# Performance work log

Measured on AMD Instinct MI355X. Metric: run time of the kernel, lower is better.

## Reference

```python
import jax, jax.numpy as jnp
import numpy as np

B, S, D, H, DFF = 2, 2048, 768, 12, 3072
DH = D // H
EPS = 1e-5


def _ln(x, g, b):
    m = jnp.mean(x, axis=-1, keepdims=True)
    v = jnp.mean((x - m) ** 2, axis=-1, keepdims=True)
    return (x - m) * jax.lax.rsqrt(v + EPS) * g + b


def setup_inputs() -> dict:
    key = jax.random.key(0)
    ks = jax.random.split(key, 13)
    sd = 1.0 / np.sqrt(D)
    sf = 1.0 / np.sqrt(DFF)
    return {
        "x": jax.random.normal(ks[0], (B, S, D), jnp.float32),
        "Wq": jax.random.uniform(ks[1], (D, D), jnp.float32, -sd, sd),
        "bq": jnp.zeros((D,), jnp.float32),
        "Wk": jax.random.uniform(ks[2], (D, D), jnp.float32, -sd, sd),
        "bk": jnp.zeros((D,), jnp.float32),
        "Wv": jax.random.uniform(ks[3], (D, D), jnp.float32, -sd, sd),
        "bv": jnp.zeros((D,), jnp.float32),
        "Wo": jax.random.uniform(ks[4], (D, D), jnp.float32, -sd, sd),
        "bo": jnp.zeros((D,), jnp.float32),
        "W1": jax.random.uniform(ks[5], (D, DFF), jnp.float32, -sd, sd),
        "b1": jnp.zeros((DFF,), jnp.float32),
        "W2": jax.random.uniform(ks[6], (DFF, D), jnp.float32, -sf, sf),
        "b2": jnp.zeros((D,), jnp.float32),
        "g1": jnp.ones((D,), jnp.float32),
        "be1": jnp.zeros((D,), jnp.float32),
        "g2": jnp.ones((D,), jnp.float32),
        "be2": jnp.zeros((D,), jnp.float32),
    }


def reference(x, Wq, bq, Wk, bk, Wv, bv, Wo, bo, W1, b1, W2, b2, g1, be1, g2, be2):
    # QKV projections, then split heads: [B,S,D] -> [B,H,S,DH]
    def heads(t):
        return t.reshape(B, S, H, DH).transpose(0, 2, 1, 3)
    Q = heads(x @ Wq + bq)
    K = heads(x @ Wk + bk)
    V = heads(x @ Wv + bv)
    # Per-head loop in original == batched-over-heads attention here (same math)
    scores = jnp.einsum("bhqd,bhkd->bhqk", Q, K) / np.sqrt(DH)
    attn = jax.nn.softmax(scores, axis=-1)  # [B,H,S,S] -- dominant intermediate
    ctx = jnp.einsum("bhqk,bhkd->bhqd", attn, V)
    ctx = ctx.transpose(0, 2, 1, 3).reshape(B, S, D)  # concat heads
    x = x + (ctx @ Wo + bo)
    x = _ln(x, g1, be1)
    ffn = (jax.nn.gelu(x @ W1 + b1, approximate=False)) @ W2 + b2
    x = _ln(x + ffn, g2, be2)
    return x
```

## Files before the change

### kernel.cpp

```cpp
#include <hip/hip_runtime.h>
#include <math.h>

#define BB 2
#define SS 2048
#define DD 768
#define HH 12
#define DHH 64
#define DFFN 3072
#define MTOK (BB*SS)
#define KVSPL 4

typedef __attribute__((ext_vector_type(8))) __bf16 bf16x8;
typedef __attribute__((ext_vector_type(4))) float f32x4;
typedef __attribute__((ext_vector_type(16))) float f32x16;

__device__ __forceinline__ unsigned short f2bf(float f) {
    unsigned int b = __builtin_bit_cast(unsigned int, f);
    b += 0x7FFFu + ((b >> 16) & 1u);
    return (unsigned short)(b >> 16);
}
__device__ __forceinline__ float bf2f(unsigned short u) {
    unsigned int b = ((unsigned int)u) << 16;
    return __builtin_bit_cast(float, b);
}

__device__ __forceinline__ void gload_lds16(const void* g, void* l) {
    __builtin_amdgcn_global_load_lds((const __attribute__((address_space(1))) unsigned int*)g,
                                     (__attribute__((address_space(3))) unsigned int*)l,
                                     16, 0, 0);
}

#if __has_builtin(__builtin_amdgcn_permlane32_swap)
#define HAVE_PSWAP 1
__device__ __forceinline__ void pswap(unsigned int x, unsigned int y,
                                      unsigned int& r0, unsigned int& r1) {
    auto r = __builtin_amdgcn_permlane32_swap(x, y, false, false);
    r0 = r[0]; r1 = r[1];
}
#else
#define HAVE_PSWAP 0
__device__ __forceinline__ void pswap(unsigned int x, unsigned int y,
                                      unsigned int& r0, unsigned int& r1) {
    unsigned int xs = __shfl_xor(x, 32);
    unsigned int ys = __shfl_xor(y, 32);
    bool hi = (threadIdx.x & 32) != 0;
    r0 = hi ? ys : x;
    r1 = hi ? y : xs;
}
#endif

__device__ __forceinline__ float xhalf_max(float v) {
    unsigned int u = __builtin_bit_cast(unsigned int, v);
    unsigned int a, b;
    pswap(u, u, a, b);
    return fmaxf(__builtin_bit_cast(float, a), __builtin_bit_cast(float, b));
}
__device__ __forceinline__ float xhalf_sum(float v) {
    unsigned int u = __builtin_bit_cast(unsigned int, v);
    unsigned int a, b;
    pswap(u, u, a, b);
    return __builtin_bit_cast(float, a) + __builtin_bit_cast(float, b);
}

template <int ACT, int OBF>
__global__ __launch_bounds__(256) void gemm_mfma(const unsigned short* __restrict__ A,
                                                 const unsigned short* __restrict__ Bt,
                                                 const float* __restrict__ bias,
                                                 void* __restrict__ Cout,
                                                 int M, int N, int ldA, int ldB, int Klen) {
    __shared__ unsigned short As[2 * 128 * 64];
    __shared__ unsigned short Bs[2 * 128 * 64];
    const int tid = threadIdx.x;
    const int lane = tid & 63;
    const int w = tid >> 6;
    const int l15 = lane & 15, l4 = lane >> 4;
    const int m0 = blockIdx.x * 128;
    const int n0 = blockIdx.y * 128;
    const int z = blockIdx.z;
    const int wr = (w >> 1) * 64;
    const int wc = (w & 1) * 64;

    const unsigned short* Az = A + (size_t)z * Klen;
    const unsigned short* Bz = Bt + (size_t)z * Klen;

    f32x4 acc[4][4] = {};

    int srow[4], scd[4];
#pragma unroll
    for (int i = 0; i < 4; ++i) {
        int s = w * 256 + i * 64 + lane;
        srow[i] = s >> 3;
        scd[i] = (((s & 7) ^ (srow[i] & 7))) * 8;
    }

#pragma unroll
    for (int i = 0; i < 4; ++i) {
        gload_lds16(Az + (size_t)(m0 + srow[i]) * ldA + scd[i], &As[(w * 256 + i * 64) * 8]);
        gload_lds16(Bz + (size_t)(n0 + srow[i]) * ldB + scd[i], &Bs[(w * 256 + i * 64) * 8]);
    }
    __syncthreads();

    int cb = 0;
    for (int k0 = 0; k0 < Klen; k0 += 64) {
        if (k0 + 64 < Klen) {
            const int nb = (cb ^ 1) * 128 * 64;
#pragma unroll
            for (int i = 0; i < 4; ++i) {
                gload_lds16(Az + (size_t)(m0 + srow[i]) * ldA + k0 + 64 + scd[i],
                            &As[nb + (w * 256 + i * 64) * 8]);
                gload_lds16(Bz + (size_t)(n0 + srow[i]) * ldB + k0 + 64 + scd[i],
                            &Bs[nb + (w * 256 + i * 64) * 8]);
            }
        }
        const unsigned short* Ac = &As[cb * 128 * 64];
        const unsigned short* Bc = &Bs[cb * 128 * 64];
#pragma unroll
        for (int ks = 0; ks < 2; ++ks) {
            bf16x8 af[4], bfr[4];
#pragma unroll
            for (int m = 0; m < 4; ++m) {
                int r = wr + m * 16 + l15;
                int c = (ks * 4 + l4) ^ (r & 7);
                af[m] = *(const bf16x8*)&Ac[(r * 8 + c) * 8];
            }
#pragma unroll
            for (int n = 0; n < 4; ++n) {
                int r = wc + n * 16 + l15;
                int c = (ks * 4 + l4) ^ (r & 7);
                bfr[n] = *(const bf16x8*)&Bc[(r * 8 + c) * 8];
            }
#pragma unroll
            for (int m = 0; m < 4; ++m)
#pragma unroll
                for (int n = 0; n < 4; ++n)
                    acc[m][n] = __builtin_amdgcn_mfma_f32_16x16x32_bf16(af[m], bfr[n], acc[m][n], 0, 0, 0);
        }
        __syncthreads();
        cb ^= 1;
    }

    const size_t zoff = (size_t)z * M * N;
#pragma unroll
    for (int n = 0; n < 4; ++n) {
        int col = n0 + wc + n * 16 + l15;
        float bv = bias ? bias[col] : 0.0f;
#pragma unroll
        for (int m = 0; m < 4; ++m) {
#pragma unroll
            for (int r = 0; r < 4; ++r) {
                int row = m0 + wr + m * 16 + l4 * 4 + r;
                float v = acc[m][n][r] + bv;
                if (ACT) v = 0.5f * v * (1.0f + erff(v * 0.70710678118654752f));
                if (OBF) ((unsigned short*)Cout)[(size_t)row * N + col] = f2bf(v);
                else     ((float*)Cout)[zoff + (size_t)row * N + col] = v;
            }
        }
    }
}

__global__ __launch_bounds__(256) void attn_mfma4(const unsigned short* __restrict__ QKV,
                                                  const unsigned short* __restrict__ Vt,
                                                  unsigned short* __restrict__ Opart,
                                                  float* __restrict__ ML) {
    __shared__ unsigned short Ks[2 * 64 * 64];
    __shared__ unsigned short Vs[2 * 64 * 64];
    const int tid = threadIdx.x;
    const int lane = tid & 63;
    const int w = tid >> 6;
    const int l31 = lane & 31;
    const int hi = lane >> 5;
    const int bh = blockIdx.y;
    const int b = bh / HH, h = bh % HH;
    const int z = blockIdx.z;
    const int q0 = blockIdx.x * 128 + w * 32;
    const float CLOG = 0.18033688011112042f;

    bf16x8 qf[4];
    {
        const unsigned short* qp = QKV + (size_t)(b * SS + q0 + l31) * 2304 + h * 64 + hi * 8;
        qf[0] = *(const bf16x8*)qp;
        qf[1] = *(const bf16x8*)(qp + 16);
        qf[2] = *(const bf16x8*)(qp + 32);
        qf[3] = *(const bf16x8*)(qp + 48);
    }

    f32x16 oacc[2] = {};
    float m_run = -1e30f, l_run = 0.0f;

    int arow[2], acd[2];
#pragma unroll
    for (int i = 0; i < 2; ++i) {
        int s = w * 128 + i * 64 + lane;
        arow[i] = s >> 3;
        acd[i] = ((s & 7) ^ (arow[i] & 7)) * 8;
    }

    const int kbase = z * (SS / KVSPL);
#pragma unroll
    for (int i = 0; i < 2; ++i) {
        gload_lds16(QKV + (size_t)(b * SS + kbase + arow[i]) * 2304 + DD + h * 64 + acd[i],
                    &Ks[(w * 128 + i * 64) * 8]);
        gload_lds16(Vt + (size_t)(bh * 64 + arow[i]) * SS + kbase + acd[i],
                    &Vs[(w * 128 + i * 64) * 8]);
    }
    __syncthreads();

    int cb = 0;
    const int NT = (SS / KVSPL) / 64;
    for (int it = 0; it < NT; ++it) {
        if (it + 1 < NT) {
            const int k0n = kbase + (it + 1) * 64;
            const int nb = (cb ^ 1) * 64 * 64;
#pragma unroll
            for (int i = 0; i < 2; ++i) {
                gload_lds16(QKV + (size_t)(b * SS + k0n + arow[i]) * 2304 + DD + h * 64 + acd[i],
                            &Ks[nb + (w * 128 + i * 64) * 8]);
                gload_lds16(Vt + (size_t)(bh * 64 + arow[i]) * SS + k0n + acd[i],
                            &Vs[nb + (w * 128 + i * 64) * 8]);
            }
        }
        const unsigned short* Kc = &Ks[cb * 64 * 64];
        const unsigned short* Vc = &Vs[cb * 64 * 64];

        f32x16 st[2] = {};
#pragma unroll
        for (int t = 0; t < 2; ++t) {
#pragma unroll
            for (int ks = 0; ks < 4; ++ks) {
                int row = 32 * t + l31;
                int ch = (2 * ks + hi) ^ (row & 7);
                bf16x8 kf = *(const bf16x8*)&Kc[(row * 8 + ch) * 8];
                st[t] = __builtin_amdgcn_mfma_f32_32x32x16_bf16(kf, qf[ks], st[t], 0, 0, 0);
            }
        }

        float pmax = st[0][0];
#pragma unroll
        for (int r = 1; r < 16; ++r) pmax = fmaxf(pmax, st[0][r]);
#pragma unroll
        for (int r = 0; r < 16; ++r) pmax = fmaxf(pmax, st[1][r]);
        pmax = xhalf_max(pmax) * CLOG;

        if (!__all(pmax <= m_run + 8.0f)) {
            float mn = fmaxf(m_run, pmax);
            float corr = exp2f(m_run - mn);
#pragma unroll
            for (int d = 0; d < 2; ++d)
#pragma unroll
                for (int r = 0; r < 16; ++r) oacc[d][r] *= corr;
            l_run *= corr;
            m_run = mn;
        }

        unsigned int Wn[2][4][2];
        float rs = 0.0f;
#pragma unroll
        for (int t = 0; t < 2; ++t) {
#pragma unroll
            for (int blk = 0; blk < 4; ++blk) {
                float pa = exp2f(fmaf(st[t][4 * blk + 0], CLOG, -m_run));
                float pb = exp2f(fmaf(st[t][4 * blk + 1], CLOG, -m_run));
                float pc = exp2f(fmaf(st[t][4 * blk + 2], CLOG, -m_run));
                float pd = exp2f(fmaf(st[t][4 * blk + 3], CLOG, -m_run));
                rs += (pa + pb) + (pc + pd);
                Wn[t][blk][0] = (unsigned int)f2bf(pa) | ((unsigned int)f2bf(pb) << 16);
                Wn[t][blk][1] = (unsigned int)f2bf(pc) | ((unsigned int)f2bf(pd) << 16);
            }
        }
        l_run += xhalf_sum(rs);

#pragma unroll
        for (int t = 0; t < 2; ++t) {
#pragma unroll
            for (int ks2 = 0; ks2 < 2; ++ks2) {
                unsigned int a0, a1, b0, b1;
                pswap(Wn[t][2 * ks2][0], Wn[t][2 * ks2 + 1][0], a0, a1);
                pswap(Wn[t][2 * ks2][1], Wn[t][2 * ks2 + 1][1], b0, b1);
                union { unsigned int u[4]; bf16x8 v; } pu;
                pu.u[0] = a0; pu.u[1] = b0;
                pu.u[2] = a1; pu.u[3] = b1;
#pragma unroll
                for (int d = 0; d < 2; ++d) {
                    int row = 32 * d + l31;
                    int ch = (4 * t + 2 * ks2 + hi) ^ (row & 7);
                    bf16x8 vf = *(const bf16x8*)&Vc[(row * 8 + ch) * 8];
                    oacc[d] = __builtin_amdgcn_mfma_f32_32x32x16_bf16(vf, pu.v, oacc[d], 0, 0, 0);
                }
            }
        }
        __syncthreads();
        cb ^= 1;
    }

    unsigned short* op = Opart + (size_t)z * MTOK * DD + (size_t)(b * SS + q0 + l31) * DD + h * 64;
#pragma unroll
    for (int d = 0; d < 2; ++d) {
#pragma unroll
        for (int blk = 0; blk < 4; ++blk) {
            unsigned long long pk =
                  (unsigned long long)f2bf(oacc[d][4 * blk + 0])
                | ((unsigned long long)f2bf(oacc[d][4 * blk + 1]) << 16)
                | ((unsigned long long)f2bf(oacc[d][4 * blk + 2]) << 32)
                | ((unsigned long long)f2bf(oacc[d][4 * blk + 3]) << 48);
            *(unsigned long long*)(op + 32 * d + 8 * blk + 4 * hi) = pk;
        }
    }
    if (hi == 0) {
        size_t mi = (((size_t)z * BB * HH + bh) * SS + (q0 + l31)) * 2;
        ML[mi] = m_run;
        ML[mi + 1] = l_run;
    }
}

__global__ __launch_bounds__(256) void attn_combine(const unsigned short* __restrict__ Opart,
                                                    const float* __restrict__ ML,
                                                    unsigned short* __restrict__ Ctx) {
    const int row = blockIdx.x;
    const int tid = threadIdx.x;
    const int b = row >> 11, s = row & 2047;
    unsigned short* co = Ctx + (size_t)row * DD;
#pragma unroll
    for (int i = 0; i < 3; ++i) {
        int c = tid + i * 256;
        int h = c >> 6;
        float m[KVSPL], l[KVSPL];
        float M = -1e30f;
#pragma unroll
        for (int zz = 0; zz < KVSPL; ++zz) {
            size_t mi = (((size_t)zz * BB * HH + b * HH + h) * SS + s) * 2;
            m[zz] = ML[mi]; l[zz] = ML[mi + 1];
            M = fmaxf(M, m[zz]);
        }
        float denom = 0.0f, num = 0.0f;
#pragma unroll
        for (int zz = 0; zz < KVSPL; ++zz) {
            float wgt = exp2f(m[zz] - M);
            denom += wgt * l[zz];
            num += wgt * bf2f(Opart[(size_t)zz * MTOK * DD + (size_t)row * DD + c]);
        }
        co[c] = f2bf(num / denom);
    }
}

__global__ __launch_bounds__(256) void v_transpose(const unsigned short* __restrict__ QKV,
                                                   unsigned short* __restrict__ Vt) {
    __shared__ unsigned short t[64][66];
    const int tid = threadIdx.x;
    const int bh = blockIdx.y, b = bh / HH, h = bh % HH;
    const int s0 = blockIdx.x * 64;
    const int c = tid & 63, r0 = tid >> 6;
#pragma unroll
    for (int i = 0; i < 16; ++i) {
        int r = i * 4 + r0;
        t[r][c] = QKV[(size_t)(b * SS + s0 + r) * 2304 + 1536 + h * 64 + c];
    }
    __syncthreads();
#pragma unroll
    for (int i = 0; i < 16; ++i) {
        int r = i * 4 + r0;
        Vt[((size_t)bh * 64 + r) * SS + s0 + c] = t[c][r];
    }
}

__global__ __launch_bounds__(256) void wtrans(const float* __restrict__ W,
                                              unsigned short* __restrict__ Wt,
                                              int K, int N, int rowoff) {
    __shared__ float t[32][33];
    const int tid = threadIdx.x;
    const int k0 = blockIdx.x * 32, n0 = blockIdx.y * 32;
    const int c = tid & 31, r0 = tid >> 5;
#pragma unroll
    for (int i = 0; i < 4; ++i) {
        int r = i * 8 + r0;
        t[r][c] = W[(size_t)(k0 + r) * N + n0 + c];
    }
    __syncthreads();
#pragma unroll
    for (int i = 0; i < 4; ++i) {
        int r = i * 8 + r0;
        Wt[(size_t)(rowoff + n0 + r) * K + k0 + c] = f2bf(t[c][r]);
    }
}

__global__ __launch_bounds__(256) void f2b_vec(const float* __restrict__ in,
                                               unsigned short* __restrict__ out, int n4) {
    int i = blockIdx.x * 256 + threadIdx.x;
    if (i < n4) {
        float4 v = ((const float4*)in)[i];
        unsigned long long pk = (unsigned long long)f2bf(v.x)
                              | ((unsigned long long)f2bf(v.y) << 16)
                              | ((unsigned long long)f2bf(v.z) << 32)
                              | ((unsigned long long)f2bf(v.w) << 48);
        ((unsigned long long*)out)[i] = pk;
    }
}

__global__ __launch_bounds__(256) void bias_concat(const float* __restrict__ q,
                                                   const float* __restrict__ k,
                                                   const float* __restrict__ v,
                                                   float* __restrict__ o) {
    int i = blockIdx.x * 256 + threadIdx.x;
    if (i < DD) { o[i] = q[i]; o[DD + i] = k[i]; o[2 * DD + i] = v[i]; }
}

template <int WB>
__global__ __launch_bounds__(256) void add_ln3(const float* __restrict__ a,
                                               const float* __restrict__ p1,
                                               const float* __restrict__ p2,
                                               const float* __restrict__ bias,
                                               const float* __restrict__ g,
                                               const float* __restrict__ be,
                                               float* __restrict__ outf,
                                               unsigned short* __restrict__ outb) {
    const int row = blockIdx.x;
    const int tid = threadIdx.x;
    float x[3];
    float s = 0.0f, s2 = 0.0f;
#pragma unroll
    for (int i = 0; i < 3; ++i) {
        int c = tid + i * 256;
        size_t idx = (size_t)row * DD + c;
        float v = a[idx] + p1[idx] + p2[idx] + bias[c];
        x[i] = v; s += v; s2 += v * v;
    }
#pragma unroll
    for (int off = 32; off; off >>= 1) {
        s += __shfl_down(s, off);
        s2 += __shfl_down(s2, off);
    }
    __shared__ float ws[8];
    const int wid = tid >> 6, lane = tid & 63;
    if (lane == 0) { ws[wid] = s; ws[4 + wid] = s2; }
    __syncthreads();
    if (tid == 0) {
        ws[0] = ws[0] + ws[1] + ws[2] + ws[3];
        ws[4] = ws[4] + ws[5] + ws[6] + ws[7];
    }
    __syncthreads();
    const float mean = ws[0] * (1.0f / DD);
    const float var = ws[4] * (1.0f / DD) - mean * mean;
    const float inv = rsqrtf(var + 1e-5f);
#pragma unroll
    for (int i = 0; i < 3; ++i) {
        int c = tid + i * 256;
        float res = (x[i] - mean) * inv * g[c] + be[c];
        outf[(size_t)row * DD + c] = res;
        if (WB) outb[(size_t)row * DD + c] = f2bf(res);
    }
}

extern "C" void kernel_launch(void* const* d_in, const int* in_sizes, int n_in,
                              void* d_out, int out_size, void* d_ws, size_t ws_size,
                              hipStream_t stream) {
    const float* x   = (const float*)d_in[0];
    const float* Wq  = (const float*)d_in[1];
    const float* bq  = (const float*)d_in[2];
    const float* Wk  = (const float*)d_in[3];
    const float* bk  = (const float*)d_in[4];
    const float* Wv  = (const float*)d_in[5];
    const float* bv  = (const float*)d_in[6];
    const float* Wo  = (const float*)d_in[7];
    const float* bo  = (const float*)d_in[8];
    const float* W1  = (const float*)d_in[9];
    const float* b1  = (const float*)d_in[10];
    const float* W2  = (const float*)d_in[11];
    const float* b2  = (const float*)d_in[12];
    const float* g1  = (const float*)d_in[13];
    const float* be1 = (const float*)d_in[14];
    const float* g2  = (const float*)d_in[15];
    const float* be2 = (const float*)d_in[16];
    float* out = (float*)d_out;

    char* w8 = (char*)d_ws;
    unsigned short* QKV = (unsigned short*)w8;
    unsigned short* Hff = (unsigned short*)w8;
    unsigned short* Vt  = (unsigned short*)(w8 + 18874368);
    unsigned short* Ctxb  = (unsigned short*)(w8 + 25165824);
    unsigned short* xb    = (unsigned short*)(w8 + 31457280);
    unsigned short* Wqkvt = (unsigned short*)(w8 + 37748736);
    unsigned short* Wot   = (unsigned short*)(w8 + 41287680);
    unsigned short* W1t   = (unsigned short*)(w8 + 42467328);
    unsigned short* W2t   = (unsigned short*)(w8 + 47185920);
    float* bqkv = (float*)(w8 + 51904512);
    unsigned short* Ob = (unsigned short*)(w8 + 51916800);
    float* Pa   = (float*)(w8 + 51916800);
    float* Pb   = (float*)(w8 + 64499712);
    float* X2   = (float*)(w8 + 77082624);
    float* ML   = (float*)(w8 + 89665536);

    dim3 blk(256);

    f2b_vec<<<dim3(3072), blk, 0, stream>>>(x, xb, MTOK * DD / 4);
    wtrans<<<dim3(24, 24), blk, 0, stream>>>(Wq, Wqkvt, DD, DD, 0);
    wtrans<<<dim3(24, 24), blk, 0, stream>>>(Wk, Wqkvt, DD, DD, DD);
    wtrans<<<dim3(24, 24), blk, 0, stream>>>(Wv, Wqkvt, DD, DD, 2 * DD);
    wtrans<<<dim3(24, 24), blk, 0, stream>>>(Wo, Wot, DD, DD, 0);
    wtrans<<<dim3(24, 96), blk, 0, stream>>>(W1, W1t, DD, DFFN, 0);
    wtrans<<<dim3(96, 24), blk, 0, stream>>>(W2, W2t, DFFN, DD, 0);
    bias_concat<<<dim3(3), blk, 0, stream>>>(bq, bk, bv, bqkv);

    gemm_mfma<0, 1><<<dim3(32, 18, 1), blk, 0, stream>>>(xb, Wqkvt, bqkv, QKV,
                                                         MTOK, 3 * DD, DD, DD, DD);
    v_transpose<<<dim3(32, 24), blk, 0, stream>>>(QKV, Vt);
    attn_mfma4<<<dim3(SS / 128, BB * HH, KVSPL), blk, 0, stream>>>(QKV, Vt, Ob, ML);
    attn_combine<<<dim3(MTOK), blk, 0, stream>>>(Ob, ML, Ctxb);
    gemm_mfma<0, 0><<<dim3(32, 6, 2), blk, 0, stream>>>(Ctxb, Wot, nullptr, Pa,
                                                        MTOK, DD, DD, DD, 384);
    add_ln3<1><<<dim3(MTOK), blk, 0, stream>>>(x, Pa, Pb, bo, g1, be1, X2, xb);
    gemm_mfma<1, 1><<<dim3(32, 24, 1), blk, 0, stream>>>(xb, W1t, b1, Hff,
                                                         MTOK, DFFN, DD, DD, DD);
    gemm_mfma<0, 0><<<dim3(32, 6, 2), blk, 0, stream>>>(Hff, W2t, nullptr, Pa,
                                                        MTOK, DD, DFFN, DFFN, 1536);
    add_ln3<0><<<dim3(MTOK), blk, 0, stream>>>(X2, Pa, Pb, b2, g2, be2, out, nullptr);
}
```

Baseline: 345.2 us.

## Merge prep kernels into one launch and use hardware bf16 pack conversion

Folds the x-to-bf16 conversion, six weight transposes and the bias concat into a single prep_all kernel, dispatched by block index, which removes seven kernel launches and their gaps. In the attention kernel, the manual round-to-nearest-even bf16 packing is replaced with the v_cvt_pk_bf16_f32 instruction, and the row-max reduction is reshaped into paired fmax trees to cut dependency depth. The inline asm ties the code to targets that support that instruction.

```diff
diff --git a/kernel.cpp b/kernel.cpp
--- a/kernel.cpp
+++ b/kernel.cpp
@@ -24,6 +24,12 @@
     return __builtin_bit_cast(float, b);
 }
 
+__device__ __forceinline__ unsigned int cvt_pk_bf16(float lo, float hi) {
+    unsigned int r;
+    asm("v_cvt_pk_bf16_f32 %0, %1, %2" : "=v"(r) : "v"(lo), "v"(hi));
+    return r;
+}
+
 __device__ __forceinline__ void gload_lds16(const void* g, void* l) {
     __builtin_amdgcn_global_load_lds((const __attribute__((address_space(1))) unsigned int*)g,
                                      (__attribute__((address_space(3))) unsigned int*)l,
@@ -31,14 +37,12 @@
 }
 
 #if __has_builtin(__builtin_amdgcn_permlane32_swap)
-#define HAVE_PSWAP 1
 __device__ __forceinline__ void pswap(unsigned int x, unsigned int y,
                                       unsigned int& r0, unsigned int& r1) {
     auto r = __builtin_amdgcn_permlane32_swap(x, y, false, false);
     r0 = r[0]; r1 = r[1];
 }
 #else
-#define HAVE_PSWAP 0
 __device__ __forceinline__ void pswap(unsigned int x, unsigned int y,
                                       unsigned int& r0, unsigned int& r1) {
     unsigned int xs = __shfl_xor(x, 32);
@@ -158,7 +162,7 @@
     }
 }
 
-__global__ __launch_bounds__(256) void attn_mfma4(const unsigned short* __restrict__ QKV,
+__global__ __launch_bounds__(256) void attn_mfma5(const unsigned short* __restrict__ QKV,
                                                   const unsigned short* __restrict__ Vt,
                                                   unsigned short* __restrict__ Opart,
                                                   float* __restrict__ ML) {
@@ -234,11 +238,12 @@
             }
         }
 
-        float pmax = st[0][0];
-#pragma unroll
-        for (int r = 1; r < 16; ++r) pmax = fmaxf(pmax, st[0][r]);
-#pragma unroll
-        for (int r = 0; r < 16; ++r) pmax = fmaxf(pmax, st[1][r]);
+        float pmax = fmaxf(st[0][0], fmaxf(st[0][1], st[0][2]));
+#pragma unroll
+        for (int r = 3; r < 15; r += 2) pmax = fmaxf(pmax, fmaxf(st[0][r], st[0][r + 1]));
+        pmax = fmaxf(pmax, st[0][15]);
+#pragma unroll
+        for (int r = 0; r < 16; r += 2) pmax = fmaxf(pmax, fmaxf(st[1][r], st[1][r + 1]));
         pmax = xhalf_max(pmax) * CLOG;
 
         if (!__all(pmax <= m_run + 8.0f)) {
@@ -263,8 +268,8 @@
                 float pc = exp2f(fmaf(st[t][4 * blk + 2], CLOG, -m_run));
                 float pd = exp2f(fmaf(st[t][4 * blk + 3], CLOG, -m_run));
                 rs += (pa + pb) + (pc + pd);
-                Wn[t][blk][0] = (unsigned int)f2bf(pa) | ((unsigned int)f2bf(pb) << 16);
-                Wn[t][blk][1] = (unsigned int)f2bf(pc) | ((unsigned int)f2bf(pd) << 16);
+                Wn[t][blk][0] = cvt_pk_bf16(pa, pb);
+                Wn[t][blk][1] = cvt_pk_bf16(pc, pd);
             }
         }
         l_run += xhalf_sum(rs);
@@ -297,12 +302,10 @@
     for (int d = 0; d < 2; ++d) {
 #pragma unroll
         for (int blk = 0; blk < 4; ++blk) {
-            unsigned long long pk =
-                  (unsigned long long)f2bf(oacc[d][4 * blk + 0])
-                | ((unsigned long long)f2bf(oacc[d][4 * blk + 1]) << 16)
-                | ((unsigned long long)f2bf(oacc[d][4 * blk + 2]) << 32)
-                | ((unsigned long long)f2bf(oacc[d][4 * blk + 3]) << 48);
-            *(unsigned long long*)(op + 32 * d + 8 * blk + 4 * hi) = pk;
+            unsigned int w0 = cvt_pk_bf16(oacc[d][4 * blk + 0], oacc[d][4 * blk + 1]);
+            unsigned int w1 = cvt_pk_bf16(oacc[d][4 * blk + 2], oacc[d][4 * blk + 3]);
+            *(unsigned long long*)(op + 32 * d + 8 * blk + 4 * hi) =
+                (unsigned long long)w0 | ((unsigned long long)w1 << 32);
         }
     }
     if (hi == 0) {
@@ -362,12 +365,11 @@
     }
 }
 
-__global__ __launch_bounds__(256) void wtrans(const float* __restrict__ W,
-                                              unsigned short* __restrict__ Wt,
-                                              int K, int N, int rowoff) {
-    __shared__ float t[32][33];
-    const int tid = threadIdx.x;
-    const int k0 = blockIdx.x * 32, n0 = blockIdx.y * 32;
+__device__ __forceinline__ void wtrans_body(const float* __restrict__ W,
+                                            unsigned short* __restrict__ Wt,
+                                            int K, int N, int rowoff,
+                                            int k0, int n0, int tid,
+                                            float (*t)[33]) {
     const int c = tid & 31, r0 = tid >> 5;
 #pragma unroll
     for (int i = 0; i < 4; ++i) {
@@ -382,25 +384,55 @@
     }
 }
 
-__global__ __launch_bounds__(256) void f2b_vec(const float* __restrict__ in,
-                                               unsigned short* __restrict__ out, int n4) {
-    int i = blockIdx.x * 256 + threadIdx.x;
-    if (i < n4) {
-        float4 v = ((const float4*)in)[i];
+__global__ __launch_bounds__(256) void prep_all(const float* __restrict__ x,
+                                                unsigned short* __restrict__ xb,
+                                                const float* __restrict__ Wq,
+                                                const float* __restrict__ Wk,
+                                                const float* __restrict__ Wv,
+                                                const float* __restrict__ Wo,
+                                                const float* __restrict__ W1,
+                                                const float* __restrict__ W2,
+                                                unsigned short* __restrict__ Wqkvt,
+                                                unsigned short* __restrict__ Wot,
+                                                unsigned short* __restrict__ W1t,
+                                                unsigned short* __restrict__ W2t,
+                                                const float* __restrict__ bq,
+                                                const float* __restrict__ bk,
+                                                const float* __restrict__ bv,
+                                                float* __restrict__ bqkv) {
+    __shared__ float t[32][33];
+    const int bid = blockIdx.x;
+    const int tid = threadIdx.x;
+    if (bid < 3072) {
+        int i = bid * 256 + tid;
+        float4 v = ((const float4*)x)[i];
         unsigned long long pk = (unsigned long long)f2bf(v.x)
                               | ((unsigned long long)f2bf(v.y) << 16)
                               | ((unsigned long long)f2bf(v.z) << 32)
                               | ((unsigned long long)f2bf(v.w) << 48);
-        ((unsigned long long*)out)[i] = pk;
-    }
-}
-
-__global__ __launch_bounds__(256) void bias_concat(const float* __restrict__ q,
-                                                   const float* __restrict__ k,
-                                                   const float* __restrict__ v,
-                                                   float* __restrict__ o) {
-    int i = blockIdx.x * 256 + threadIdx.x;
-    if (i < DD) { o[i] = q[i]; o[DD + i] = k[i]; o[2 * DD + i] = v[i]; }
+        ((unsigned long long*)xb)[i] = pk;
+    } else if (bid < 3648) {
+        int lb = bid - 3072;
+        wtrans_body(Wq, Wqkvt, DD, DD, 0, (lb % 24) * 32, (lb / 24) * 32, tid, t);
+    } else if (bid < 4224) {
+        int lb = bid - 3648;
+        wtrans_body(Wk, Wqkvt, DD, DD, DD, (lb % 24) * 32, (lb / 24) * 32, tid, t);
+    } else if (bid < 4800) {
+        int lb = bid - 4224;
+        wtrans_body(Wv, Wqkvt, DD, DD, 2 * DD, (lb % 24) * 32, (lb / 24) * 32, tid, t);
+    } else if (bid < 5376) {
+        int lb = bid - 4800;
+        wtrans_body(Wo, Wot, DD, DD, 0, (lb % 24) * 32, (lb / 24) * 32, tid, t);
+    } else if (bid < 7680) {
+        int lb = bid - 5376;
+        wtrans_body(W1, W1t, DD, DFFN, 0, (lb % 24) * 32, (lb / 24) * 32, tid, t);
+    } else if (bid < 9984) {
+        int lb = bid - 7680;
+        wtrans_body(W2, W2t, DFFN, DD, 0, (lb % 96) * 32, (lb / 96) * 32, tid, t);
+    } else {
+        int i = (bid - 9984) * 256 + tid;
+        if (i < DD) { bqkv[i] = bq[i]; bqkv[DD + i] = bk[i]; bqkv[2 * DD + i] = bv[i]; }
+    }
 }
 
 template <int WB>
@@ -490,19 +522,13 @@
 
     dim3 blk(256);
 
-    f2b_vec<<<dim3(3072), blk, 0, stream>>>(x, xb, MTOK * DD / 4);
-    wtrans<<<dim3(24, 24), blk, 0, stream>>>(Wq, Wqkvt, DD, DD, 0);
-    wtrans<<<dim3(24, 24), blk, 0, stream>>>(Wk, Wqkvt, DD, DD, DD);
-    wtrans<<<dim3(24, 24), blk, 0, stream>>>(Wv, Wqkvt, DD, DD, 2 * DD);
-    wtrans<<<dim3(24, 24), blk, 0, stream>>>(Wo, Wot, DD, DD, 0);
-    wtrans<<<dim3(24, 96), blk, 0, stream>>>(W1, W1t, DD, DFFN, 0);
-    wtrans<<<dim3(96, 24), blk, 0, stream>>>(W2, W2t, DFFN, DD, 0);
-    bias_concat<<<dim3(3), blk, 0, stream>>>(bq, bk, bv, bqkv);
+    prep_all<<<dim3(9987), blk, 0, stream>>>(x, xb, Wq, Wk, Wv, Wo, W1, W2,
+                                             Wqkvt, Wot, W1t, W2t, bq, bk, bv, bqkv);
 
     gemm_mfma<0, 1><<<dim3(32, 18, 1), blk, 0, stream>>>(xb, Wqkvt, bqkv, QKV,
                                                          MTOK, 3 * DD, DD, DD, DD);
     v_transpose<<<dim3(32, 24), blk, 0, stream>>>(QKV, Vt);
-    attn_mfma4<<<dim3(SS / 128, BB * HH, KVSPL), blk, 0, stream>>>(QKV, Vt, Ob, ML);
+    attn_mfma5<<<dim3(SS / 128, BB * HH, KVSPL), blk, 0, stream>>>(QKV, Vt, Ob, ML);
     attn_combine<<<dim3(MTOK), blk, 0, stream>>>(Ob, ML, Ctxb);
     gemm_mfma<0, 0><<<dim3(32, 6, 2), blk, 0, stream>>>(Ctxb, Wot, nullptr, Pa,
                                                         MTOK, DD, DD, DD, 384);
```

Result: faster. 333.6 us (-3.3%).
